# Kernel tuning notes

Hardware: AMD Instinct MI355X
Metric: run time of the kernel (lower is better)

## Reference

```python
import jax, jax.numpy as jnp
import numpy as np

N = 200000   # total nodes
E = 800000   # total edges
G = 4096     # number of graphs
DIM_DRUG = 78
GNN = 128


def batch_norm(x, g, b, m, v):
    # eval-mode BatchNorm1d
    return (x - m) * jax.lax.rsqrt(v + 1e-5) * g + b


def gin_conv(x, edge_index, w1, b1, w2, b2):
    # PyG GINConv, eps=0: out = MLP((1+eps)*x + sum_{j->i} x_j)
    agg = jax.ops.segment_sum(x[edge_index[0]], edge_index[1], num_segments=N)
    h = x + agg
    return jax.nn.relu(h @ w1 + b1) @ w2 + b2


def gcn_conv(x, edge_index, w, b):
    # PyG GCNConv with added self-loops and symmetric normalization
    xw = x @ w  # [N, out]
    loop = jnp.arange(N, dtype=edge_index.dtype)
    src = jnp.concatenate([edge_index[0], loop])
    dst = jnp.concatenate([edge_index[1], loop])
    deg = jax.ops.segment_sum(jnp.ones_like(dst, dtype=xw.dtype), dst, num_segments=N)
    dinv = jnp.where(deg > 0, deg ** -0.5, 0.0)
    msg = xw[src] * (dinv[src] * dinv[dst])[:, None]
    return jax.ops.segment_sum(msg, dst, num_segments=N) + b


def segment_softmax(scores, seg):
    m = jax.ops.segment_max(scores, seg, num_segments=G)
    e = jnp.exp(scores - m[seg])
    z = jax.ops.segment_sum(e, seg, num_segments=G)
    return e / z[seg]


def sag_pool(x, edge_index, batch, gcn_w, gcn_b):
    scores = jnp.tanh(gcn_conv(x, edge_index, gcn_w, gcn_b)[:, 0])
    norm = segment_softmax(scores, batch)
    pooled = jax.ops.segment_sum(x * norm[:, None], batch, num_segments=G)
    return pooled


def setup_inputs() -> dict:
    key = jax.random.key(0)
    ks = jax.random.split(key, 24)
    d = {}
    d['drug_feature'] = jax.random.normal(ks[0], (N, DIM_DRUG), jnp.float32)
    d['edge_index'] = jax.random.randint(ks[1], (2, E), 0, N, jnp.int64 if jax.config.jax_enable_x64 else jnp.int32)
    d['ibatch'] = jnp.sort(jax.random.randint(ks[2], (N,), 0, G, jnp.int32))
    # BatchNorm params (eval mode)
    d['bn0_g'] = jax.random.uniform(ks[3], (DIM_DRUG,), jnp.float32, 0.5, 1.5)
    d['bn0_b'] = jax.random.normal(ks[4], (DIM_DRUG,)) * 0.1
    d['bn0_m'] = jax.random.normal(ks[5], (DIM_DRUG,)) * 0.1
    d['bn0_v'] = jax.random.uniform(ks[6], (DIM_DRUG,), jnp.float32, 0.5, 1.5)
    d['bn1_g'] = jax.random.uniform(ks[7], (GNN,), jnp.float32, 0.5, 1.5)
    d['bn1_b'] = jax.random.normal(ks[8], (GNN,)) * 0.1
    d['bn1_m'] = jax.random.normal(ks[9], (GNN,)) * 0.1
    d['bn1_v'] = jax.random.uniform(ks[10], (GNN,), jnp.float32, 0.5, 1.5)
    d['bn2_g'] = jax.random.uniform(ks[11], (GNN,), jnp.float32, 0.5, 1.5)
    d['bn2_b'] = jax.random.normal(ks[12], (GNN,)) * 0.1
    d['bn2_m'] = jax.random.normal(ks[13], (GNN,)) * 0.1
    d['bn2_v'] = jax.random.uniform(ks[14], (GNN,), jnp.float32, 0.5, 1.5)
    # GIN MLPs
    s1 = (2.0 / DIM_DRUG) ** 0.5
    d['gin1_w1'] = jax.random.normal(ks[15], (DIM_DRUG, 2 * GNN)) * s1
    d['gin1_b1'] = jnp.zeros((2 * GNN,), jnp.float32)
    d['gin1_w2'] = jax.random.normal(ks[16], (2 * GNN, GNN)) * (2.0 / (2 * GNN)) ** 0.5
    d['gin1_b2'] = jnp.zeros((GNN,), jnp.float32)
    d['gin2_w1'] = jax.random.normal(ks[17], (GNN, 2 * GNN)) * (2.0 / GNN) ** 0.5
    d['gin2_b1'] = jnp.zeros((2 * GNN,), jnp.float32)
    d['gin2_w2'] = jax.random.normal(ks[18], (2 * GNN, GNN)) * (2.0 / (2 * GNN)) ** 0.5
    d['gin2_b2'] = jnp.zeros((GNN,), jnp.float32)
    # SAG pooling GCN scorers (out_channels=1)
    d['gcn1_w'] = jax.random.normal(ks[19], (GNN, 1)) * (1.0 / GNN) ** 0.5
    d['gcn1_b'] = jnp.zeros((1,), jnp.float32)
    d['gcn2_w'] = jax.random.normal(ks[20], (GNN, 1)) * (1.0 / GNN) ** 0.5
    d['gcn2_b'] = jnp.zeros((1,), jnp.float32)
    return d


def reference(drug_feature, bn0_g, bn0_b, bn0_m, bn0_v,
              gin1_w1, gin1_b1, gin1_w2, gin1_b2, bn1_g, bn1_b, bn1_m, bn1_v,
              gin2_w1, gin2_b1, gin2_w2, gin2_b2, bn2_g, bn2_b, bn2_m, bn2_v,
              gcn1_w, gcn1_b, gcn2_w, gcn2_b, edge_index, ibatch):
    x = batch_norm(drug_feature, bn0_g, bn0_b, bn0_m, bn0_v)
    h1 = gin_conv(x, edge_index, gin1_w1, gin1_b1, gin1_w2, gin1_b2)
    h1 = batch_norm(jax.nn.relu(h1), bn1_g, bn1_b, bn1_m, bn1_v)  # dropout = identity (eval)
    h2 = gin_conv(h1, edge_index, gin2_w1, gin2_b1, gin2_w2, gin2_b2)
    h2 = batch_norm(jax.nn.relu(h2), bn2_g, bn2_b, bn2_m, bn2_v)
    g1 = sag_pool(h1, edge_index, ibatch, gcn1_w, gcn1_b)
    g2 = sag_pool(h2, edge_index, ibatch, gcn2_w, gcn2_b)
    return jnp.stack((g1, g2), axis=1)  # [G, 2, GNN]
```

## Files before the change

### kernel.cpp

```cpp
#include <hip/hip_runtime.h>
#include <hip/hip_bf16.h>

typedef __hip_bfloat16 bf16;
typedef __attribute__((ext_vector_type(8))) short short8;
typedef __attribute__((ext_vector_type(4))) float f32x4;

#define NN 200000
#define EE 800000
#define GG 4096
#define DD 78
#define HH 128
#define CAP 24
#define ZR NN

__device__ __forceinline__ float b2f(bf16 x) { return __bfloat162float(x); }
__device__ __forceinline__ bf16 f2b(float x) { return __float2bfloat16(x); }
__device__ __forceinline__ unsigned short f2u(float f) {
    bf16 h = __float2bfloat16(f);
    return __builtin_bit_cast(unsigned short, h);
}
__device__ __forceinline__ float u2f(unsigned int u) {
    return __builtin_bit_cast(float, u << 16);
}

constexpr size_t OFF_CNT   = 0;
constexpr size_t OFF_ELL   = OFF_CNT  + (size_t)NN * 4;
constexpr size_t OFF_H1    = OFF_ELL  + (size_t)NN * CAP * 4;
constexpr size_t OFF_H2    = OFF_H1   + (size_t)(NN + 64) * HH * 2;
constexpr size_t OFF_X96   = OFF_H2;
constexpr size_t OFF_DINV  = OFF_H2   + (size_t)NN * HH * 2;
constexpr size_t OFF_SP1   = OFF_DINV + (size_t)NN * 4;
constexpr size_t OFF_SP2   = OFF_SP1  + (size_t)NN * 4;
constexpr size_t OFF_E1    = OFF_SP2  + (size_t)NN * 4;
constexpr size_t OFF_E2    = OFF_E1   + (size_t)NN * 4;
constexpr size_t OFF_START = OFF_E2   + (size_t)NN * 4;
constexpr size_t OFF_P1A   = OFF_START + 16640;
constexpr size_t OFF_P1B   = OFF_P1A  + 24576 * 2;
constexpr size_t OFF_P2A   = OFF_P1B  + 32768 * 2;
constexpr size_t OFF_P2B   = OFF_P2A  + 32768 * 2;
constexpr size_t OFF_END   = OFF_P2B  + 32768 * 2;


__global__ void ell_build(const int* __restrict__ src, const int* __restrict__ dst,
                          int* __restrict__ cnt, int* __restrict__ ell) {
    int e = blockIdx.x * 256 + threadIdx.x;
    if (e >= EE) return;
    int t = dst[e];
    int slot = atomicAdd(&cnt[t], 1);
    if (slot < CAP) ell[t * CAP + slot] = src[e];
}

__global__ void dinv_kernel(const int* __restrict__ cnt, float* __restrict__ dinv,
                            bf16* __restrict__ H1) {
    int i = blockIdx.x * 256 + threadIdx.x;
    if (i < NN) dinv[i] = rsqrtf((float)cnt[i] + 1.0f);
    if (i < HH) H1[(size_t)ZR * HH + i] = f2b(0.f);
}

__global__ void start_kernel(const int* __restrict__ ibatch, int* __restrict__ startg) {
    int i = blockIdx.x * 256 + threadIdx.x;
    if (i >= NN) return;
    int b = ibatch[i];
    int pb = (i == 0) ? -1 : ibatch[i - 1];
    for (int g = pb + 1; g <= b; g++) startg[g] = i;
    if (i == NN - 1) {
        for (int g = b + 1; g <= GG; g++) startg[g] = NN;
    }
}

__global__ void x96_prep(const float* __restrict__ feat, const float* __restrict__ g,
                         const float* __restrict__ b, const float* __restrict__ m,
                         const float* __restrict__ v, bf16* __restrict__ X96) {
    int idx = blockIdx.x * 256 + threadIdx.x;
    if (idx >= (NN + 1) * 96) return;
    int row = idx / 96, col = idx - row * 96;
    float out = 0.f;
    if (row < NN && col < DD) {
        float s = g[col] * rsqrtf(v[col] + 1e-5f);
        out = feat[(size_t)row * DD + col] * s + (b[col] - m[col] * s);
    }
    X96[idx] = f2b(out);
}

__global__ void pack_w(const float* __restrict__ w, bf16* __restrict__ wp,
                       int Krows, int Ncols, int total) {
    int idx = blockIdx.x * 256 + threadIdx.x;
    if (idx >= total) return;
    int j = idx & 7;
    int l = (idx >> 3) & 63;
    int f = idx >> 9;
    int CT = Ncols >> 4;
    int ct = f % CT;
    int ks = f / CT;
    int k = ks * 32 + (l >> 4) * 8 + j;
    int n = ct * 16 + (l & 15);
    float val = (k < Krows) ? w[(size_t)k * Ncols + n] : 0.0f;
    wp[idx] = f2b(val);
}

template <int K, int KS1>
__launch_bounds__(256, 4)
__global__ void gin_mfma(const bf16* __restrict__ xin,
                         const int* __restrict__ ell, const int* __restrict__ cnt,
                         const bf16* __restrict__ pA, const float* __restrict__ b1,
                         const bf16* __restrict__ pB, const float* __restrict__ b2,
                         const float* __restrict__ bng, const float* __restrict__ bnb,
                         const float* __restrict__ bnm, const float* __restrict__ bnv,
                         const float* __restrict__ gcnw,
                         bf16* __restrict__ hout, float* __restrict__ SP) {
    __shared__ short hld[32][K + 8];
    __shared__ short hid[32][264];
    const int tid  = threadIdx.x;
    const int lane = tid & 63;
    const int w    = tid >> 6;
    const int l15  = lane & 15;
    const int q4   = lane >> 4;
    const int row0 = blockIdx.x * 32;

    if (K == 128 || l15 < 12) {
        const int qd = l15 * 8;
        const short* base = (const short*)xin;
#pragma unroll
        for (int t = 0; t < 2; t++) {
            const int lr = w * 8 + t * 4 + q4;
            const int node = row0 + lr;
            int c_raw = cnt[node];
            int4 sA = *(const int4*)(ell + node * CAP + 0);
            int4 sB = *(const int4*)(ell + node * CAP + 4);
            uint4 u = *(const uint4*)(base + (size_t)node * K + qd);
            int c = c_raw > CAP ? CAP : c_raw;
            float a0 = u2f(u.x), a1 = u2f(u.x >> 16);
            float a2 = u2f(u.y), a3 = u2f(u.y >> 16);
            float a4 = u2f(u.z), a5 = u2f(u.z >> 16);
            float a6 = u2f(u.w), a7 = u2f(u.w >> 16);
            int i0 = (c > 0) ? sA.x : ZR;
            int i1 = (c > 1) ? sA.y : ZR;
            int i2 = (c > 2) ? sA.z : ZR;
            int i3 = (c > 3) ? sA.w : ZR;
            int i4 = (c > 4) ? sB.x : ZR;
            int i5 = (c > 5) ? sB.y : ZR;
            int i6 = (c > 6) ? sB.z : ZR;
            int i7 = (c > 7) ? sB.w : ZR;
            uint4 u0 = *(const uint4*)(base + (size_t)i0 * K + qd);
            uint4 u1 = *(const uint4*)(base + (size_t)i1 * K + qd);
            uint4 u2 = *(const uint4*)(base + (size_t)i2 * K + qd);
            uint4 u3 = *(const uint4*)(base + (size_t)i3 * K + qd);
            uint4 u4 = *(const uint4*)(base + (size_t)i4 * K + qd);
            uint4 u5 = *(const uint4*)(base + (size_t)i5 * K + qd);
            uint4 u6 = *(const uint4*)(base + (size_t)i6 * K + qd);
            uint4 u7 = *(const uint4*)(base + (size_t)i7 * K + qd);
            a0 += u2f(u0.x) + u2f(u1.x) + u2f(u2.x) + u2f(u3.x)
                + u2f(u4.x) + u2f(u5.x) + u2f(u6.x) + u2f(u7.x);
            a1 += u2f(u0.x >> 16) + u2f(u1.x >> 16) + u2f(u2.x >> 16) + u2f(u3.x >> 16)
                + u2f(u4.x >> 16) + u2f(u5.x >> 16) + u2f(u6.x >> 16) + u2f(u7.x >> 16);
            a2 += u2f(u0.y) + u2f(u1.y) + u2f(u2.y) + u2f(u3.y)
                + u2f(u4.y) + u2f(u5.y) + u2f(u6.y) + u2f(u7.y);
            a3 += u2f(u0.y >> 16) + u2f(u1.y >> 16) + u2f(u2.y >> 16) + u2f(u3.y >> 16)
                + u2f(u4.y >> 16) + u2f(u5.y >> 16) + u2f(u6.y >> 16) + u2f(u7.y >> 16);
            a4 += u2f(u0.z) + u2f(u1.z) + u2f(u2.z) + u2f(u3.z)
                + u2f(u4.z) + u2f(u5.z) + u2f(u6.z) + u2f(u7.z);
            a5 += u2f(u0.z >> 16) + u2f(u1.z >> 16) + u2f(u2.z >> 16) + u2f(u3.z >> 16)
                + u2f(u4.z >> 16) + u2f(u5.z >> 16) + u2f(u6.z >> 16) + u2f(u7.z >> 16);
            a6 += u2f(u0.w) + u2f(u1.w) + u2f(u2.w) + u2f(u3.w)
                + u2f(u4.w) + u2f(u5.w) + u2f(u6.w) + u2f(u7.w);
            a7 += u2f(u0.w >> 16) + u2f(u1.w >> 16) + u2f(u2.w >> 16) + u2f(u3.w >> 16)
                + u2f(u4.w >> 16) + u2f(u5.w >> 16) + u2f(u6.w >> 16) + u2f(u7.w >> 16);
            for (int kk = 8; kk < c; kk += 4) {
                int4 ss = *(const int4*)(ell + node * CAP + kk);
                int s0 = ss.x;
                int s1 = (kk + 1 < c) ? ss.y : ZR;
                int s2 = (kk + 2 < c) ? ss.z : ZR;
                int s3 = (kk + 3 < c) ? ss.w : ZR;
                uint4 v0 = *(const uint4*)(base + (size_t)s0 * K + qd);
                uint4 v1 = *(const uint4*)(base + (size_t)s1 * K + qd);
                uint4 v2 = *(const uint4*)(base + (size_t)s2 * K + qd);
                uint4 v3 = *(const uint4*)(base + (size_t)s3 * K + qd);
                a0 += u2f(v0.x) + u2f(v1.x) + u2f(v2.x) + u2f(v3.x);
                a1 += u2f(v0.x >> 16) + u2f(v1.x >> 16) + u2f(v2.x >> 16) + u2f(v3.x >> 16);
                a2 += u2f(v0.y) + u2f(v1.y) + u2f(v2.y) + u2f(v3.y);
                a3 += u2f(v0.y >> 16) + u2f(v1.y >> 16) + u2f(v2.y >> 16) + u2f(v3.y >> 16);
                a4 += u2f(v0.z) + u2f(v1.z) + u2f(v2.z) + u2f(v3.z);
                a5 += u2f(v0.z >> 16) + u2f(v1.z >> 16) + u2f(v2.z >> 16) + u2f(v3.z >> 16);
                a6 += u2f(v0.w) + u2f(v1.w) + u2f(v2.w) + u2f(v3.w);
                a7 += u2f(v0.w >> 16) + u2f(v1.w >> 16) + u2f(v2.w >> 16) + u2f(v3.w >> 16);
            }
            uint4 o;
            o.x = (unsigned)f2u(a0) | ((unsigned)f2u(a1) << 16);
            o.y = (unsigned)f2u(a2) | ((unsigned)f2u(a3) << 16);
            o.z = (unsigned)f2u(a4) | ((unsigned)f2u(a5) << 16);
            o.w = (unsigned)f2u(a6) | ((unsigned)f2u(a7) << 16);
            *(uint4*)&hld[lr][qd] = o;
        }
    }
    __syncthreads();

    {
        f32x4 acc[2][4];
#pragma unroll
        for (int ct = 0; ct < 4; ct++) {
            float bv = b1[w * 64 + ct * 16 + l15];
            acc[0][ct] = (f32x4){bv, bv, bv, bv};
            acc[1][ct] = (f32x4){bv, bv, bv, bv};
        }
#pragma unroll
        for (int ks = 0; ks < KS1; ks++) {
            short8 fa0 = *(const short8*)&hld[l15][ks * 32 + q4 * 8];
            short8 fa1 = *(const short8*)&hld[16 + l15][ks * 32 + q4 * 8];
#pragma unroll
            for (int ct = 0; ct < 4; ct++) {
                int cg = w * 4 + ct;
                short8 fb = *(const short8*)((const short*)pA + (((size_t)(ks * 16 + cg) * 64 + lane) << 3));
                acc[0][ct] = __builtin_amdgcn_mfma_f32_16x16x32_bf16(fa0, fb, acc[0][ct], 0, 0, 0);
                acc[1][ct] = __builtin_amdgcn_mfma_f32_16x16x32_bf16(fa1, fb, acc[1][ct], 0, 0, 0);
            }
        }
#pragma unroll
        for (int rt = 0; rt < 2; rt++)
#pragma unroll
            for (int ct = 0; ct < 4; ct++)
#pragma unroll
                for (int r = 0; r < 4; r++) {
                    int row = rt * 16 + q4 * 4 + r;
                    int col = w * 64 + ct * 16 + l15;
                    hid[row][col] = (short)f2u(fmaxf(acc[rt][ct][r], 0.0f));
                }
    }
    __syncthreads();

    {
        f32x4 acc2[2][2];
#pragma unroll
        for (int ct = 0; ct < 2; ct++) {
            float bv = b2[w * 32 + ct * 16 + l15];
            acc2[0][ct] = (f32x4){bv, bv, bv, bv};
            acc2[1][ct] = (f32x4){bv, bv, bv, bv};
        }
#pragma unroll
        for (int ks = 0; ks < 8; ks++) {
            short8 fa0 = *(const short8*)&hid[l15][ks * 32 + q4 * 8];
            short8 fa1 = *(const short8*)&hid[16 + l15][ks * 32 + q4 * 8];
#pragma unroll
            for (int ct = 0; ct < 2; ct++) {
                int cg = w * 2 + ct;
                short8 fb = *(const short8*)((const short*)pB + (((size_t)(ks * 8 + cg) * 64 + lane) << 3));
                acc2[0][ct] = __builtin_amdgcn_mfma_f32_16x16x32_bf16(fa0, fb, acc2[0][ct], 0, 0, 0);
                acc2[1][ct] = __builtin_amdgcn_mfma_f32_16x16x32_bf16(fa1, fb, acc2[1][ct], 0, 0, 0);
            }
        }
        float p[2][4] = {{0.f, 0.f, 0.f, 0.f}, {0.f, 0.f, 0.f, 0.f}};
#pragma unroll
        for (int ct = 0; ct < 2; ct++) {
            int col = w * 32 + ct * 16 + l15;
            float s  = bng[col] * rsqrtf(bnv[col] + 1e-5f);
            float sh = bnb[col] - bnm[col] * s;
            float gw = gcnw[col];
#pragma unroll
            for (int rt = 0; rt < 2; rt++)
#pragma unroll
                for (int r = 0; r < 4; r++) {
                    float vv = fmaxf(acc2[rt][ct][r], 0.0f) * s + sh;
                    int row = rt * 16 + q4 * 4 + r;
                    hout[(size_t)(row0 + row) * HH + col] = f2b(vv);
                    p[rt][r] += vv * gw;
                }
        }
#pragma unroll
        for (int rt = 0; rt < 2; rt++)
#pragma unroll
            for (int r = 0; r < 4; r++) {
                float v = p[rt][r];
                v += __shfl_xor(v, 1);
                v += __shfl_xor(v, 2);
                v += __shfl_xor(v, 4);
                v += __shfl_xor(v, 8);
                if (l15 == 0) atomicAdd(&SP[row0 + rt * 16 + q4 * 4 + r], v);
            }
    }
}


__global__ void finalize_kernel(const float* __restrict__ sp1, const float* __restrict__ sp2,
                                const float* __restrict__ dinv,
                                const int* __restrict__ ell, const int* __restrict__ cnt,
                                const float* __restrict__ gb1, const float* __restrict__ gb2,
                                float* __restrict__ e1, float* __restrict__ e2) {
    int i = blockIdx.x * 256 + threadIdx.x;
    if (i >= NN) return;
    float di = dinv[i];
    int c = cnt[i];
    if (c > CAP) c = CAP;
    float a1 = sp1[i] * di, a2 = sp2[i] * di;
    for (int k = 0; k < c; k++) {
        int s = ell[i * CAP + k];
        float f = dinv[s];
        a1 += sp1[s] * f;
        a2 += sp2[s] * f;
    }
    float sc1 = tanhf(a1 * di + gb1[0]);
    float sc2 = tanhf(a2 * di + gb2[0]);
    e1[i] = expf(sc1);
    e2[i] = expf(sc2);
}

__global__ void pool_kernel(const bf16* __restrict__ H1, const bf16* __restrict__ H2,
                            const float* __restrict__ e1, const float* __restrict__ e2,
                            const int* __restrict__ startg, float* __restrict__ out) {
    int g = blockIdx.x;
    int lo = startg[g], hi = startg[g + 1];
    int tid = threadIdx.x;

    float z1 = 0.f, z2 = 0.f;
    for (int i = lo + tid; i < hi; i += 128) { z1 += e1[i]; z2 += e2[i]; }
    __shared__ float red[256];
    red[tid] = z1; red[128 + tid] = z2;
    __syncthreads();
    if (tid == 0) {
        float a = 0.f, b = 0.f;
        for (int t = 0; t < 128; t++) { a += red[t]; b += red[128 + t]; }
        red[0] = a; red[128] = b;
    }
    __syncthreads();
    float inv1 = red[0]   > 0.f ? 1.0f / red[0]   : 0.f;
    float inv2 = red[128] > 0.f ? 1.0f / red[128] : 0.f;

    float acc1 = 0.f, acc2 = 0.f;
    for (int i = lo; i < hi; i++) {
        float w1 = e1[i], w2 = e2[i];
        acc1 += b2f(H1[(size_t)i * HH + tid]) * w1;
        acc2 += b2f(H2[(size_t)i * HH + tid]) * w2;
    }
    out[(size_t)(g * 2 + 0) * HH + tid] = acc1 * inv1;
    out[(size_t)(g * 2 + 1) * HH + tid] = acc2 * inv2;
}

__global__ void zero_out_kernel(float* __restrict__ out, int n) {
    int i = blockIdx.x * 256 + threadIdx.x;
    if (i < n) out[i] = 0.f;
}

extern "C" void kernel_launch(void* const* d_in, const int* in_sizes, int n_in,
                              void* d_out, int out_size, void* d_ws, size_t ws_size,
                              hipStream_t stream) {
    const float* feat   = (const float*)d_in[0];
    const int*   ei     = (const int*)d_in[1];
    const int*   ibatch = (const int*)d_in[2];
    const float* bn0_g = (const float*)d_in[3],  *bn0_b = (const float*)d_in[4];
    const float* bn0_m = (const float*)d_in[5],  *bn0_v = (const float*)d_in[6];
    const float* bn1_g = (const float*)d_in[7],  *bn1_b = (const float*)d_in[8];
    const float* bn1_m = (const float*)d_in[9],  *bn1_v = (const float*)d_in[10];
    const float* bn2_g = (const float*)d_in[11], *bn2_b = (const float*)d_in[12];
    const float* bn2_m = (const float*)d_in[13], *bn2_v = (const float*)d_in[14];
    const float* g1w1 = (const float*)d_in[15], *g1b1 = (const float*)d_in[16];
    const float* g1w2 = (const float*)d_in[17], *g1b2 = (const float*)d_in[18];
    const float* g2w1 = (const float*)d_in[19], *g2b1 = (const float*)d_in[20];
    const float* g2w2 = (const float*)d_in[21], *g2b2 = (const float*)d_in[22];
    const float* gcn1_w = (const float*)d_in[23], *gcn1_b = (const float*)d_in[24];
    const float* gcn2_w = (const float*)d_in[25], *gcn2_b = (const float*)d_in[26];

    float* outp = (float*)d_out;

    if (ws_size < OFF_END) {
        zero_out_kernel<<<(out_size + 255) / 256, 256, 0, stream>>>(outp, out_size);
        return;
    }

    char* ws = (char*)d_ws;
    int*   CNT    = (int*)(ws + OFF_CNT);
    int*   ELL    = (int*)(ws + OFF_ELL);
    bf16*  H1     = (bf16*)(ws + OFF_H1);
    bf16*  H2     = (bf16*)(ws + OFF_H2);
    bf16*  X96    = (bf16*)(ws + OFF_X96);
    float* DINV   = (float*)(ws + OFF_DINV);
    float* SP1    = (float*)(ws + OFF_SP1);
    float* SP2    = (float*)(ws + OFF_SP2);
    float* E1     = (float*)(ws + OFF_E1);
    float* E2     = (float*)(ws + OFF_E2);
    int*   STARTG = (int*)(ws + OFF_START);
    bf16*  P1A    = (bf16*)(ws + OFF_P1A);
    bf16*  P1B    = (bf16*)(ws + OFF_P1B);
    bf16*  P2A    = (bf16*)(ws + OFF_P2A);
    bf16*  P2B    = (bf16*)(ws + OFF_P2B);

    const int* esrc = ei;
    const int* edst = ei + EE;

    hipMemsetAsync(CNT, 0, (size_t)NN * 4, stream);
    hipMemsetAsync(SP1, 0, (size_t)2 * NN * 4, stream);

    ell_build<<<(EE + 255) / 256, 256, 0, stream>>>(esrc, edst, CNT, ELL);
    dinv_kernel<<<(NN + 255) / 256, 256, 0, stream>>>(CNT, DINV, H1);
    start_kernel<<<(NN + 255) / 256, 256, 0, stream>>>(ibatch, STARTG);

    pack_w<<<(24576 + 255) / 256, 256, 0, stream>>>(g1w1, P1A, DD,  256, 24576);
    pack_w<<<(32768 + 255) / 256, 256, 0, stream>>>(g1w2, P1B, 256, 128, 32768);
    pack_w<<<(32768 + 255) / 256, 256, 0, stream>>>(g2w1, P2A, 128, 256, 32768);
    pack_w<<<(32768 + 255) / 256, 256, 0, stream>>>(g2w2, P2B, 256, 128, 32768);

    x96_prep<<<((NN + 1) * 96 + 255) / 256, 256, 0, stream>>>(feat, bn0_g, bn0_b, bn0_m, bn0_v, X96);

    gin_mfma<96, 3><<<NN / 32, 256, 0, stream>>>(X96, ELL, CNT, P1A, g1b1, P1B, g1b2,
                                                 bn1_g, bn1_b, bn1_m, bn1_v, gcn1_w, H1, SP1);
    gin_mfma<128, 4><<<NN / 32, 256, 0, stream>>>(H1, ELL, CNT, P2A, g2b1, P2B, g2b2,
                                                  bn2_g, bn2_b, bn2_m, bn2_v, gcn2_w, H2, SP2);

    finalize_kernel<<<(NN + 255) / 256, 256, 0, stream>>>(SP1, SP2, DINV, ELL, CNT,
                                                          gcn1_b, gcn2_b, E1, E2);
    pool_kernel<<<GG, 128, 0, stream>>>(H1, H2, E1, E2, STARTG, outp);
}
```

Baseline: 299.0 us.

## Merge setup kernels, vectorize input prep, and parallelize pooling over nodes

Fuses dinv/start kernels and the four weight-packing launches into single kernels, cutting launch count. The input BN prep now writes four bf16 values per thread with a vector store, and the zero row is written elsewhere. Pool kernel now uses 256 threads, with four waves striding over the nodes and each lane handling two features via 32-bit loads, then reducing in shared memory. This replaces a serial per-node loop and a single-thread sum. NN*24/256 is exact (18750 blocks), so x96_prep needs no bounds check.

```diff
diff --git a/kernel.cpp b/kernel.cpp
--- a/kernel.cpp
+++ b/kernel.cpp
@@ -4,6 +4,7 @@
 typedef __hip_bfloat16 bf16;
 typedef __attribute__((ext_vector_type(8))) short short8;
 typedef __attribute__((ext_vector_type(4))) float f32x4;
+typedef __attribute__((ext_vector_type(4))) unsigned short u16x4;
 
 #define NN 200000
 #define EE 800000
@@ -50,42 +51,44 @@
     if (slot < CAP) ell[t * CAP + slot] = src[e];
 }
 
-__global__ void dinv_kernel(const int* __restrict__ cnt, float* __restrict__ dinv,
-                            bf16* __restrict__ H1) {
+__global__ void dinv_start(const int* __restrict__ cnt, float* __restrict__ dinv,
+                           bf16* __restrict__ H1, bf16* __restrict__ X96,
+                           const int* __restrict__ ibatch, int* __restrict__ startg) {
     int i = blockIdx.x * 256 + threadIdx.x;
     if (i < NN) dinv[i] = rsqrtf((float)cnt[i] + 1.0f);
     if (i < HH) H1[(size_t)ZR * HH + i] = f2b(0.f);
-}
-
-__global__ void start_kernel(const int* __restrict__ ibatch, int* __restrict__ startg) {
-    int i = blockIdx.x * 256 + threadIdx.x;
-    if (i >= NN) return;
-    int b = ibatch[i];
-    int pb = (i == 0) ? -1 : ibatch[i - 1];
-    for (int g = pb + 1; g <= b; g++) startg[g] = i;
-    if (i == NN - 1) {
-        for (int g = b + 1; g <= GG; g++) startg[g] = NN;
+    if (i < 96) X96[(size_t)ZR * 96 + i] = f2b(0.f);
+    if (i < NN) {
+        int b = ibatch[i];
+        int pb = (i == 0) ? -1 : ibatch[i - 1];
+        for (int g = pb + 1; g <= b; g++) startg[g] = i;
+        if (i == NN - 1) {
+            for (int g = b + 1; g <= GG; g++) startg[g] = NN;
+        }
     }
 }
 
 __global__ void x96_prep(const float* __restrict__ feat, const float* __restrict__ g,
                          const float* __restrict__ b, const float* __restrict__ m,
                          const float* __restrict__ v, bf16* __restrict__ X96) {
-    int idx = blockIdx.x * 256 + threadIdx.x;
-    if (idx >= (NN + 1) * 96) return;
-    int row = idx / 96, col = idx - row * 96;
-    float out = 0.f;
-    if (row < NN && col < DD) {
-        float s = g[col] * rsqrtf(v[col] + 1e-5f);
-        out = feat[(size_t)row * DD + col] * s + (b[col] - m[col] * s);
-    }
-    X96[idx] = f2b(out);
-}
-
-__global__ void pack_w(const float* __restrict__ w, bf16* __restrict__ wp,
-                       int Krows, int Ncols, int total) {
-    int idx = blockIdx.x * 256 + threadIdx.x;
-    if (idx >= total) return;
+    int gi = blockIdx.x * 256 + threadIdx.x;
+    int row = gi / 24;
+    int c0 = (gi - row * 24) * 4;
+    float o[4];
+#pragma unroll
+    for (int j = 0; j < 4; j++) {
+        int c = c0 + j;
+        if (c < DD) {
+            float s = g[c] * rsqrtf(v[c] + 1e-5f);
+            o[j] = feat[(size_t)row * DD + c] * s + (b[c] - m[c] * s);
+        } else o[j] = 0.f;
+    }
+    u16x4 st = {f2u(o[0]), f2u(o[1]), f2u(o[2]), f2u(o[3])};
+    *(u16x4*)((unsigned short*)X96 + (size_t)row * 96 + c0) = st;
+}
+
+__device__ __forceinline__ void pack_one(const float* __restrict__ w, bf16* __restrict__ wp,
+                                         int Krows, int Ncols, int idx) {
     int j = idx & 7;
     int l = (idx >> 3) & 63;
     int f = idx >> 9;
@@ -96,6 +99,17 @@
     int n = ct * 16 + (l & 15);
     float val = (k < Krows) ? w[(size_t)k * Ncols + n] : 0.0f;
     wp[idx] = f2b(val);
+}
+
+__global__ void pack_all(const float* __restrict__ w1a, const float* __restrict__ w1b,
+                         const float* __restrict__ w2a, const float* __restrict__ w2b,
+                         bf16* __restrict__ P1A, bf16* __restrict__ P1B,
+                         bf16* __restrict__ P2A, bf16* __restrict__ P2B) {
+    const int b = blockIdx.x, tid = threadIdx.x;
+    if (b < 96)       pack_one(w1a, P1A, DD,  256, b * 256 + tid);
+    else if (b < 224) pack_one(w1b, P1B, 256, 128, (b - 96) * 256 + tid);
+    else if (b < 352) pack_one(w2a, P2A, 128, 256, (b - 224) * 256 + tid);
+    else              pack_one(w2b, P2B, 256, 128, (b - 352) * 256 + tid);
 }
 
 template <int K, int KS1>
@@ -308,29 +322,35 @@
     int g = blockIdx.x;
     int lo = startg[g], hi = startg[g + 1];
     int tid = threadIdx.x;
-
+    int w = tid >> 6, l = tid & 63;
+
+    float acc1[2] = {0.f, 0.f}, acc2[2] = {0.f, 0.f};
     float z1 = 0.f, z2 = 0.f;
-    for (int i = lo + tid; i < hi; i += 128) { z1 += e1[i]; z2 += e2[i]; }
-    __shared__ float red[256];
-    red[tid] = z1; red[128 + tid] = z2;
+    for (int i = lo + w; i < hi; i += 4) {
+        float e1i = e1[i], e2i = e2[i];
+        z1 += e1i; z2 += e2i;
+        unsigned h1 = *(const unsigned*)((const short*)H1 + (size_t)i * HH + l * 2);
+        unsigned h2 = *(const unsigned*)((const short*)H2 + (size_t)i * HH + l * 2);
+        acc1[0] += u2f(h1) * e1i; acc1[1] += u2f(h1 >> 16) * e1i;
+        acc2[0] += u2f(h2) * e2i; acc2[1] += u2f(h2 >> 16) * e2i;
+    }
+    __shared__ float pacc[4][128];
+    __shared__ float qacc[4][128];
+    __shared__ float zz[4][2];
+    pacc[w][l * 2 + 0] = acc1[0]; pacc[w][l * 2 + 1] = acc1[1];
+    qacc[w][l * 2 + 0] = acc2[0]; qacc[w][l * 2 + 1] = acc2[1];
+    if (l == 0) { zz[w][0] = z1; zz[w][1] = z2; }
     __syncthreads();
-    if (tid == 0) {
-        float a = 0.f, b = 0.f;
-        for (int t = 0; t < 128; t++) { a += red[t]; b += red[128 + t]; }
-        red[0] = a; red[128] = b;
-    }
-    __syncthreads();
-    float inv1 = red[0]   > 0.f ? 1.0f / red[0]   : 0.f;
-    float inv2 = red[128] > 0.f ? 1.0f / red[128] : 0.f;
-
-    float acc1 = 0.f, acc2 = 0.f;
-    for (int i = lo; i < hi; i++) {
-        float w1 = e1[i], w2 = e2[i];
-        acc1 += b2f(H1[(size_t)i * HH + tid]) * w1;
-        acc2 += b2f(H2[(size_t)i * HH + tid]) * w2;
-    }
-    out[(size_t)(g * 2 + 0) * HH + tid] = acc1 * inv1;
-    out[(size_t)(g * 2 + 1) * HH + tid] = acc2 * inv2;
+    if (tid < 128) {
+        float s  = pacc[0][tid] + pacc[1][tid] + pacc[2][tid] + pacc[3][tid];
+        float zt = zz[0][0] + zz[1][0] + zz[2][0] + zz[3][0];
+        out[(size_t)(g * 2 + 0) * HH + tid] = (zt > 0.f) ? s / zt : 0.f;
+    } else {
+        int d = tid - 128;
+        float s  = qacc[0][d] + qacc[1][d] + qacc[2][d] + qacc[3][d];
+        float zt = zz[0][1] + zz[1][1] + zz[2][1] + zz[3][1];
+        out[(size_t)(g * 2 + 1) * HH + d] = (zt > 0.f) ? s / zt : 0.f;
+    }
 }
 
 __global__ void zero_out_kernel(float* __restrict__ out, int n) {
@@ -388,15 +408,9 @@
     hipMemsetAsync(SP1, 0, (size_t)2 * NN * 4, stream);
 
     ell_build<<<(EE + 255) / 256, 256, 0, stream>>>(esrc, edst, CNT, ELL);
-    dinv_kernel<<<(NN + 255) / 256, 256, 0, stream>>>(CNT, DINV, H1);
-    start_kernel<<<(NN + 255) / 256, 256, 0, stream>>>(ibatch, STARTG);
-
-    pack_w<<<(24576 + 255) / 256, 256, 0, stream>>>(g1w1, P1A, DD,  256, 24576);
-    pack_w<<<(32768 + 255) / 256, 256, 0, stream>>>(g1w2, P1B, 256, 128, 32768);
-    pack_w<<<(32768 + 255) / 256, 256, 0, stream>>>(g2w1, P2A, 128, 256, 32768);
-    pack_w<<<(32768 + 255) / 256, 256, 0, stream>>>(g2w2, P2B, 256, 128, 32768);
-
-    x96_prep<<<((NN + 1) * 96 + 255) / 256, 256, 0, stream>>>(feat, bn0_g, bn0_b, bn0_m, bn0_v, X96);
+    dinv_start<<<(NN + 255) / 256, 256, 0, stream>>>(CNT, DINV, H1, X96, ibatch, STARTG);
+    pack_all<<<480, 256, 0, stream>>>(g1w1, g1w2, g2w1, g2w2, P1A, P1B, P2A, P2B);
+    x96_prep<<<NN * 24 / 256, 256, 0, stream>>>(feat, bn0_g, bn0_b, bn0_m, bn0_v, X96);
 
     gin_mfma<96, 3><<<NN / 32, 256, 0, stream>>>(X96, ELL, CNT, P1A, g1b1, P1B, g1b2,
                                                  bn1_g, bn1_b, bn1_m, bn1_v, gcn1_w, H1, SP1);
@@ -405,5 +419,5 @@
 
     finalize_kernel<<<(NN + 255) / 256, 256, 0, stream>>>(SP1, SP2, DINV, ELL, CNT,
                                                           gcn1_b, gcn2_b, E1, E2);
-    pool_kernel<<<GG, 128, 0, stream>>>(H1, H2, E1, E2, STARTG, outp);
-}
+    pool_kernel<<<GG, 256, 0, stream>>>(H1, H2, E1, E2, STARTG, outp);
+}
```

Measured after the change: 329.9 us. 10.3% more time.
